# Kernel tuning notes

Measured on AMD Instinct MI355X. Metric: run time of the kernel, lower is better.

## Reference

```python
import jax, jax.numpy as jnp
import numpy as np

CTX = 2048   # context_window
D   = 256    # emb_dim
B   = 16     # batch
C   = 2048   # sequence length (<= CTX)


def make_rotary_matrix(ctx, d):
    """Dense per-position rotation matrix, as in the tinyllama get_rotary_matrix:
    theta_i = 10000 ** (-2*(i-1)/d), 2x2 rotation blocks on the diagonal."""
    pos = np.arange(ctx, dtype=np.float64)[:, None]            # [ctx, 1]
    i = np.arange(d // 2, dtype=np.float64)                    # [d/2]
    theta = 10000.0 ** (-2.0 * (i - 1.0) / d)                  # note (i-1), matches source
    ang = pos * theta                                          # [ctx, d/2]
    c, s = np.cos(ang), np.sin(ang)
    R = np.zeros((ctx, d, d), dtype=np.float32)
    k = np.arange(d // 2)
    R[:, 2 * k, 2 * k] = c
    R[:, 2 * k, 2 * k + 1] = -s
    R[:, 2 * k + 1, 2 * k] = s
    R[:, 2 * k + 1, 2 * k + 1] = c
    return jnp.asarray(R)


def setup_inputs() -> dict:
    key = jax.random.key(0)
    ks = jax.random.split(key, 4)
    scale = 1.0 / np.sqrt(D)
    x = jax.random.normal(ks[0], (B, C, D), dtype=jnp.float32)
    Wq = jax.random.normal(ks[1], (D, D), dtype=jnp.float32) * scale
    Wk = jax.random.normal(ks[2], (D, D), dtype=jnp.float32) * scale
    Wv = jax.random.normal(ks[3], (D, D), dtype=jnp.float32) * scale
    bq = jnp.zeros((D,), dtype=jnp.float32)
    bk = jnp.zeros((D,), dtype=jnp.float32)
    bv = jnp.zeros((D,), dtype=jnp.float32)
    R = make_rotary_matrix(CTX, D)
    return {"x": x, "Wq": Wq, "bq": bq, "Wk": Wk, "bk": bk, "Wv": Wv, "bv": bv, "R": R}


def reference(x, Wq, bq, Wk, bk, Wv, bv, R):
    Bz, Cz, d = x.shape
    # QKV projections (torch Linear: y = x @ W.T + b)
    q = x @ Wq.T + bq
    k = x @ Wk.T + bk
    v = x @ Wv.T + bv
    # Dense rotary: q_rot[b,c,:] = R[c] @ q[b,c,:]  (original: bmm(q^T, R[:C]^T)^T)
    Rc = R[:Cz]                                        # [C, D, D]
    q_rot = jnp.einsum('bcd,ced->bce', q, Rc)          # [B, C, D]
    k_rot = jnp.einsum('bcd,ced->bce', k, Rc)          # [B, C, D]
    # Causal SDPA (dropout_p=0.2 in source -> disabled here, eval-mode determinism)
    scale = 1.0 / jnp.sqrt(jnp.asarray(d, dtype=x.dtype))
    scores = jnp.einsum('bqd,bkd->bqk', q_rot, k_rot) * scale   # [B, C, C]
    causal = jnp.tril(jnp.ones((Cz, Cz), dtype=bool))
    scores = jnp.where(causal, scores, jnp.asarray(-jnp.inf, dtype=scores.dtype))
    attn = jax.nn.softmax(scores, axis=-1)
    out = jnp.einsum('bqk,bkd->bqd', attn, v)                   # [B, C, D]
    return out
```

## Files before the change

kernel.cpp:

```cpp
#include <hip/hip_runtime.h>
#include <stdint.h>

#define BB 16
#define CC 2048
#define DD 256
#define MM (BB*CC)

typedef __attribute__((ext_vector_type(4))) float f32x4;
typedef __attribute__((ext_vector_type(8))) short bf16x8;
typedef __attribute__((ext_vector_type(4))) short s16x4;

static __device__ __forceinline__ short f2bf(float f) {
  union { float f; uint32_t u; } v; v.f = f;
  uint32_t u = v.u;
  return (short)((u + 0x7FFFu + ((u >> 16) & 1u)) >> 16);
}

#define GLDS16(gp, lp) __builtin_amdgcn_global_load_lds(                      \
    (const __attribute__((address_space(1))) void*)(gp),                      \
    (__attribute__((address_space(3))) void*)(lp), 16, 0, 0)

#define DPP_ROR_F(x, n) __uint_as_float(__builtin_amdgcn_update_dpp(          \
    0, (int)__float_as_uint(x), 0x120 + (n), 0xF, 0xF, false))

__global__ __launch_bounds__(256) void k_trig(float2* __restrict__ cs) {
  int id = blockIdx.x * 256 + threadIdx.x;
  int k = id & 127, pg = id >> 7;
  double th = pow(10000.0, (1.0 - (double)k) * (1.0 / 128.0));
  const double TWO_PI = 6.283185307179586476925287;
  const double INV_2PI = 1.0 / TWO_PI;
  #pragma unroll
  for (int i = 0; i < 16; ++i) {
    int pos = pg * 16 + i;
    double ang = (double)pos * th;
    double red = ang - floor(ang * INV_2PI) * TWO_PI;
    float fr = (float)red;
    cs[(size_t)pos * 128 + k] = make_float2(__cosf(fr), __sinf(fr));
  }
}

__global__ __launch_bounds__(256) void k_wconv(
    const float* __restrict__ Wq, const float* __restrict__ Wk,
    const float* __restrict__ Wv, short* __restrict__ wb) {
  int gid = blockIdx.x * 256 + threadIdx.x;
  int mat = gid >> 14;
  int rem = gid & 16383;
  int kc = rem >> 11;
  int o  = (rem & 2047) * 8;
  int e  = o >> 6;
  int c4 = ((o & 63) ^ (((e >> 1) & 3) << 4)) >> 3;
  const float* W = (mat == 0) ? Wq : (mat == 1) ? Wk : Wv;
  f32x4 wv = *(const f32x4*)(W + (size_t)e * DD + kc * 32 + c4 * 4);
  s16x4 b4;
  b4[0] = f2bf(wv[0]); b4[1] = f2bf(wv[1]); b4[2] = f2bf(wv[2]); b4[3] = f2bf(wv[3]);
  *(s16x4*)((char*)wb + (size_t)gid * 8) = b4;
}

__global__ __launch_bounds__(256, 2) void k_qkv(
    const float* __restrict__ x, const short* __restrict__ wb,
    const float* __restrict__ bq, const float* __restrict__ bk,
    const float* __restrict__ bv, const float2* __restrict__ cs,
    short* __restrict__ q_rot, short* __restrict__ k_rot,
    short* __restrict__ v_t)
{
  __shared__ char SM[32768 + 49152];
  short* xs = (short*)SM;
  char* wsh = SM + 32768;
  const int t = threadIdx.x;
  const int lane = t & 63, w = t >> 6;
  const int g = lane >> 4, li = lane & 15;
  const int m0 = blockIdx.x * 64;

  #pragma unroll
  for (int i = 0; i < 16; ++i) {
    int chunk = i * 256 + t;
    int row = chunk >> 6, c4 = chunk & 63;
    f32x4 xv = *(const f32x4*)(x + (size_t)(m0 + row) * DD + c4 * 4);
    s16x4 b4;
    b4[0] = f2bf(xv[0]); b4[1] = f2bf(xv[1]); b4[2] = f2bf(xv[2]); b4[3] = f2bf(xv[3]);
    *(s16x4*)((char*)xs + row * 512 + ((c4 * 8) ^ ((row & 7) << 4))) = b4;
  }
  __syncthreads();

  f32x4 zero4 = {0.f, 0.f, 0.f, 0.f};
  f32x4 accQ[16], accK[16], accV[16];
  #pragma unroll
  for (int nt = 0; nt < 16; ++nt) { accQ[nt] = zero4; accK[nt] = zero4; accV[nt] = zero4; }

  for (int kc = 0; kc < 8; ++kc) {
    #pragma unroll
    for (int i = 0; i < 12; ++i) {
      int cc = i * 4 + w;
      const char* src = (const char*)wb + (size_t)(cc >> 4) * 131072 +
                        kc * 16384 + (cc & 15) * 1024 + lane * 16;
      GLDS16(src, wsh + cc * 1024);
    }
    asm volatile("s_waitcnt vmcnt(0)" ::: "memory");
    __builtin_amdgcn_sched_barrier(0);
    __builtin_amdgcn_s_barrier();

    const int arow = w * 16 + li;
    bf16x8 a = *(const bf16x8*)((char*)xs + arow * 512 +
                                (((kc * 64) + g * 16) ^ ((arow & 7) << 4)));
    #pragma unroll
    for (int nt = 0; nt < 16; ++nt) {
      int e = nt * 16 + li;
      int off = e * 64 + ((g * 16) ^ (((e >> 1) & 3) << 4));
      bf16x8 fq = *(const bf16x8*)(wsh + off);
      bf16x8 fk = *(const bf16x8*)(wsh + 16384 + off);
      bf16x8 fv = *(const bf16x8*)(wsh + 32768 + off);
      accQ[nt] = __builtin_amdgcn_mfma_f32_16x16x32_bf16(a, fq, accQ[nt], 0, 0, 0);
      accK[nt] = __builtin_amdgcn_mfma_f32_16x16x32_bf16(a, fk, accK[nt], 0, 0, 0);
      accV[nt] = __builtin_amdgcn_mfma_f32_16x16x32_bf16(a, fv, accV[nt], 0, 0, 0);
    }
    __builtin_amdgcn_s_barrier();
  }

  __syncthreads();
  {
    char* Tq = SM;
    char* Tk = SM + 33792;
    #pragma unroll
    for (int nt = 0; nt < 16; ++nt) {
      int e = nt * 16 + li;
      float bQ = bq[e], bK = bk[e];
      #pragma unroll
      for (int r = 0; r < 4; ++r) {
        int cloc = w * 16 + g * 4 + r;
        int m = m0 + cloc;
        float2 csv = cs[(size_t)(m & (CC - 1)) * 128 + (e >> 1)];
        float vq = accQ[nt][r] + bQ;
        float oq = __shfl_xor(vq, 1);
        vq = csv.x * vq + ((e & 1) ? csv.y * oq : -csv.y * oq);
        *(short*)(Tq + cloc * 528 + e * 2) = f2bf(vq * 0.0625f);
        float vk = accK[nt][r] + bK;
        float ok = __shfl_xor(vk, 1);
        vk = csv.x * vk + ((e & 1) ? csv.y * ok : -csv.y * ok);
        *(short*)(Tk + cloc * 528 + e * 2) = f2bf(vk);
      }
    }
    __syncthreads();
    #pragma unroll
    for (int it = 0; it < 8; ++it) {
      int chunk = it * 256 + t;
      int c = chunk >> 5, e32 = chunk & 31;
      int4 vq4 = *(const int4*)(Tq + c * 528 + e32 * 16);
      int4 vk4 = *(const int4*)(Tk + c * 528 + e32 * 16);
      *(int4*)(q_rot + (size_t)(m0 + c) * DD + e32 * 8) = vq4;
      *(int4*)(k_rot + (size_t)(m0 + c) * DD + e32 * 8) = vk4;
    }
  }
  __syncthreads();
  #pragma unroll
  for (int nt = 0; nt < 16; ++nt) {
    int e = nt * 16 + li;
    float bias = bv[e];
    #pragma unroll
    for (int r = 0; r < 4; ++r) {
      int cloc = w * 16 + g * 4 + r;
      *(short*)(SM + e * 144 + cloc * 2) = f2bf(accV[nt][r] + bias);
    }
  }
  __syncthreads();
  {
    const int bb = m0 >> 11, c0 = m0 & (CC - 1);
    #pragma unroll
    for (int it = 0; it < 8; ++it) {
      int chunk = it * 256 + t;
      int e = chunk >> 3, c8 = chunk & 7;
      int4 vv = *(const int4*)(SM + e * 144 + c8 * 16);
      *(int4*)(v_t + ((size_t)(bb * DD + e)) * CC + c0 + c8 * 8) = vv;
    }
  }
}

__global__ __launch_bounds__(512, 2) void k_attn(
    const short* __restrict__ q_rot, const short* __restrict__ k_rot,
    const short* __restrict__ v_t, float* __restrict__ out)
{
  __shared__ char SM[143360];
  const int t = threadIdx.x;
  const int lane = t & 63, w = t >> 6;
  const int wg = w & 3, gq = w >> 2;
  const int g = lane >> 4, li = lane & 15;

  const int p = blockIdx.x;
  const int b = p & 15;
  const int j = p >> 4;

  const short* kbase = k_rot + (size_t)b * CC * DD;
  const short* vbase = v_t  + (size_t)b * DD * CC;

  float* U  = (float*)(SM + 65536);
  float* ML = (float*)(SM + 142848);
  char* Pb = SM + 132608 + w * 1280;

  f32x4 zero4 = {0.f, 0.f, 0.f, 0.f};

  for (int tt = 0; tt < 2; ++tt) {
    const int qt = tt ? (31 - j) : j;
    const int q0 = qt * 64;
    const int NTg = qt + 1;
    const int kvoff = gq * 32 * NTg;

    const short* qb = q_rot + ((size_t)b * CC + q0 + wg * 16 + li) * DD;
    bf16x8 qf[8];
    #pragma unroll
    for (int dc = 0; dc < 8; ++dc)
      qf[dc] = *(const bf16x8*)(qb + dc * 32 + g * 8);

    f32x4 O[16];
    #pragma unroll
    for (int i = 0; i < 16; ++i) O[i] = zero4;
    float mrow[4], lrow[4];
    #pragma unroll
    for (int r = 0; r < 4; ++r) { mrow[r] = -__builtin_inff(); lrow[r] = 0.f; }

    auto STAGE = [&](int buf, int kt) {
      const int k0s = kvoff + kt * 32;
      char* dst = SM + (size_t)(gq * 2 + buf) * 32768;
      #pragma unroll
      for (int i = 0; i < 4; ++i) {
        int c = i * 4 + wg;
        int row = 2 * c + (lane >> 5);
        int cb = ((lane & 31) * 16) ^ ((row & 7) << 4);
        const char* src = (const char*)(kbase + (size_t)(k0s + row) * DD) + cb;
        GLDS16(src, dst + c * 1024);
      }
      #pragma unroll
      for (int i = 0; i < 4; ++i) {
        int c = i * 4 + wg;
        int d = 16 * c + (lane >> 2);
        int sb = (((lane & 3) ^ ((lane >> 3) & 3)) * 16);
        const char* src = (const char*)(vbase + (size_t)d * CC + k0s) + sb;
        GLDS16(src, dst + 16384 + c * 1024);
      }
    };

    int cur = 0;
    STAGE(0, 0);
    for (int kt = 0; kt < NTg; ++kt) {
      const int k0 = kvoff + kt * 32;
      if (kt + 1 < NTg) {
        STAGE(cur ^ 1, kt + 1);
        asm volatile("s_waitcnt vmcnt(8)" ::: "memory");
      } else {
        asm volatile("s_waitcnt vmcnt(0)" ::: "memory");
      }
      __builtin_amdgcn_sched_barrier(0);
      __builtin_amdgcn_s_barrier();

      const char* Kb = SM + (size_t)(gq * 2 + cur) * 32768;
      const char* Vb = Kb + 16384;

      f32x4 S[2];
      S[0] = zero4; S[1] = zero4;
      __builtin_amdgcn_s_setprio(1);
      #pragma unroll
      for (int dc = 0; dc < 8; ++dc) {
        #pragma unroll
        for (int nt = 0; nt < 2; ++nt) {
          int krow = nt * 16 + li;
          bf16x8 kf = *(const bf16x8*)(Kb + krow * 512 +
                                       (((dc * 64) + g * 16) ^ ((krow & 7) << 4)));
          S[nt] = __builtin_amdgcn_mfma_f32_16x16x32_bf16(qf[dc], kf, S[nt], 0, 0, 0);
        }
      }
      __builtin_amdgcn_s_setprio(0);

      if (k0 + 31 > q0) {
        #pragma unroll
        for (int nt = 0; nt < 2; ++nt)
          #pragma unroll
          for (int r = 0; r < 4; ++r)
            if ((k0 + nt * 16 + li) > (q0 + wg * 16 + g * 4 + r))
              S[nt][r] = -1.0e30f;
      }

      float mxr[4];
      #pragma unroll
      for (int r = 0; r < 4; ++r) {
        float mx = fmaxf(S[0][r], S[1][r]);
        mx = fmaxf(mx, DPP_ROR_F(mx, 8));
        mx = fmaxf(mx, DPP_ROR_F(mx, 4));
        mx = fmaxf(mx, DPP_ROR_F(mx, 2));
        mx = fmaxf(mx, DPP_ROR_F(mx, 1));
        mxr[r] = mx;
      }
      int need = 0;
      #pragma unroll
      for (int r = 0; r < 4; ++r) need |= (mxr[r] > mrow[r] + 8.f) ? 1 : 0;
      if (__any(need)) {
        #pragma unroll
        for (int r = 0; r < 4; ++r) {
          float mnew = fmaxf(mrow[r], mxr[r]);
          float al = __expf(mrow[r] - mnew);
          mrow[r] = mnew;
          lrow[r] *= al;
          #pragma unroll
          for (int dt2 = 0; dt2 < 16; ++dt2) O[dt2][r] *= al;
        }
      }
      #pragma unroll
      for (int r = 0; r < 4; ++r) {
        float rsum = 0.f;
        #pragma unroll
        for (int nt = 0; nt < 2; ++nt) {
          float pv = __expf(S[nt][r] - mrow[r]);
          S[nt][r] = pv;
          rsum += pv;
        }
        rsum += DPP_ROR_F(rsum, 8);
        rsum += DPP_ROR_F(rsum, 4);
        rsum += DPP_ROR_F(rsum, 2);
        rsum += DPP_ROR_F(rsum, 1);
        lrow[r] += rsum;
      }

      #pragma unroll
      for (int nt = 0; nt < 2; ++nt)
        #pragma unroll
        for (int r = 0; r < 4; ++r)
          *(short*)(Pb + (g * 4 + r) * 80 + (nt * 16 + li) * 2) = f2bf(S[nt][r]);

      bf16x8 pf = *(const bf16x8*)(Pb + li * 80 + g * 16);

      __builtin_amdgcn_s_setprio(1);
      #pragma unroll
      for (int dt2 = 0; dt2 < 16; ++dt2) {
        bf16x8 vf = *(const bf16x8*)(Vb + (dt2 * 16 + li) * 64 +
                                     ((g * 16) ^ ((((li) >> 1) & 3) << 4)));
        O[dt2] = __builtin_amdgcn_mfma_f32_16x16x32_bf16(pf, vf, O[dt2], 0, 0, 0);
      }
      __builtin_amdgcn_s_setprio(0);

      __builtin_amdgcn_s_barrier();
      cur ^= 1;
    }

    __syncthreads();
    if (gq == 1) {
      #pragma unroll
      for (int r = 0; r < 4; ++r) {
        int row = wg * 16 + g * 4 + r;
        if (li == 0) { ML[row * 2] = mrow[r]; ML[row * 2 + 1] = lrow[r]; }
        #pragma unroll
        for (int dt2 = 0; dt2 < 16; ++dt2)
          U[row * 260 + dt2 * 16 + li] = O[dt2][r];
      }
    }
    __syncthreads();
    if (gq == 0) {
      float eA[4], eB[4], invl[4];
      #pragma unroll
      for (int r = 0; r < 4; ++r) {
        int row = wg * 16 + g * 4 + r;
        float mB = ML[row * 2], lB = ML[row * 2 + 1];
        float m = fmaxf(mrow[r], mB);
        eA[r] = __expf(mrow[r] - m);
        eB[r] = __expf(mB - m);
        invl[r] = 1.f / (lrow[r] * eA[r] + lB * eB[r]);
      }
      #pragma unroll
      for (int dt2 = 0; dt2 < 16; ++dt2)
        #pragma unroll
        for (int r = 0; r < 4; ++r) {
          int row = wg * 16 + g * 4 + r;
          float uB = U[row * 260 + dt2 * 16 + li];
          out[((size_t)b * CC + q0 + row) * DD + dt2 * 16 + li] =
              (O[dt2][r] * eA[r] + uB * eB[r]) * invl[r];
        }
    }
    __syncthreads();
  }
}

extern "C" void kernel_launch(void* const* d_in, const int* in_sizes, int n_in,
                              void* d_out, int out_size, void* d_ws, size_t ws_size,
                              hipStream_t stream) {
  const float* x  = (const float*)d_in[0];
  const float* Wq = (const float*)d_in[1];
  const float* bq = (const float*)d_in[2];
  const float* Wk = (const float*)d_in[3];
  const float* bk = (const float*)d_in[4];
  const float* Wv = (const float*)d_in[5];
  const float* bv = (const float*)d_in[6];
  float* out = (float*)d_out;
  (void)in_sizes; (void)n_in; (void)out_size; (void)ws_size;

  char* ws = (char*)d_ws;
  float2* cs   = (float2*)ws;
  short* q_rot = (short*)(ws + (2u << 20));
  short* k_rot = q_rot + (size_t)MM * DD;
  short* v_tr  = k_rot + (size_t)MM * DD;
  short* wb    = v_tr + (size_t)MM * DD;

  k_trig <<<  64, 256, 0, stream>>>(cs);
  k_wconv<<< 192, 256, 0, stream>>>(Wq, Wk, Wv, wb);
  k_qkv  <<< 512, 256, 0, stream>>>(x, wb, bq, bk, bv, cs, q_rot, k_rot, v_tr);
  k_attn <<< 256, 512, 0, stream>>>(q_rot, k_rot, v_tr, out);
}
```

Measured before the change: 129.3 us.

## Split QKV projection across six waves, one matrix per wave pair

The QKV kernel grows from 4 to 6 waves per block. Each pair of waves owns one of Q, K, V and computes 32 rows by 256 columns, instead of each wave computing all three matrices for 16 rows. This cuts accumulator registers per wave (32 instead of 48 f32x4) and reuses each weight fragment across two row blocks. The LDS-staged transpose and store epilogue is replaced by direct scattered 2-byte global stores for q/k and 8-byte stores for v_t, which drops barriers but may lower store coalescing.

```diff
diff --git a/kernel.cpp b/kernel.cpp
--- a/kernel.cpp
+++ b/kernel.cpp
@@ -56,7 +56,7 @@
   *(s16x4*)((char*)wb + (size_t)gid * 8) = b4;
 }
 
-__global__ __launch_bounds__(256, 2) void k_qkv(
+__global__ __launch_bounds__(384, 2) void k_qkv(
     const float* __restrict__ x, const short* __restrict__ wb,
     const float* __restrict__ bq, const float* __restrict__ bk,
     const float* __restrict__ bv, const float2* __restrict__ cs,
@@ -68,29 +68,34 @@
   char* wsh = SM + 32768;
   const int t = threadIdx.x;
   const int lane = t & 63, w = t >> 6;
+  const int mat = w >> 1, h = w & 1;
   const int g = lane >> 4, li = lane & 15;
   const int m0 = blockIdx.x * 64;
 
   #pragma unroll
-  for (int i = 0; i < 16; ++i) {
-    int chunk = i * 256 + t;
-    int row = chunk >> 6, c4 = chunk & 63;
-    f32x4 xv = *(const f32x4*)(x + (size_t)(m0 + row) * DD + c4 * 4);
-    s16x4 b4;
-    b4[0] = f2bf(xv[0]); b4[1] = f2bf(xv[1]); b4[2] = f2bf(xv[2]); b4[3] = f2bf(xv[3]);
-    *(s16x4*)((char*)xs + row * 512 + ((c4 * 8) ^ ((row & 7) << 4))) = b4;
+  for (int i = 0; i < 11; ++i) {
+    int chunk = i * 384 + t;
+    if (chunk < 4096) {
+      int row = chunk >> 6, c4 = chunk & 63;
+      f32x4 xv = *(const f32x4*)(x + (size_t)(m0 + row) * DD + c4 * 4);
+      s16x4 b4;
+      b4[0] = f2bf(xv[0]); b4[1] = f2bf(xv[1]); b4[2] = f2bf(xv[2]); b4[3] = f2bf(xv[3]);
+      *(s16x4*)((char*)xs + row * 512 + ((c4 * 8) ^ ((row & 7) << 4))) = b4;
+    }
   }
   __syncthreads();
 
   f32x4 zero4 = {0.f, 0.f, 0.f, 0.f};
-  f32x4 accQ[16], accK[16], accV[16];
+  f32x4 acc[2][16];
   #pragma unroll
-  for (int nt = 0; nt < 16; ++nt) { accQ[nt] = zero4; accK[nt] = zero4; accV[nt] = zero4; }
+  for (int rb = 0; rb < 2; ++rb)
+    #pragma unroll
+    for (int nt = 0; nt < 16; ++nt) acc[rb][nt] = zero4;
 
   for (int kc = 0; kc < 8; ++kc) {
     #pragma unroll
-    for (int i = 0; i < 12; ++i) {
-      int cc = i * 4 + w;
+    for (int i = 0; i < 8; ++i) {
+      int cc = i * 6 + w;
       const char* src = (const char*)wb + (size_t)(cc >> 4) * 131072 +
                         kc * 16384 + (cc & 15) * 1024 + lane * 16;
       GLDS16(src, wsh + cc * 1024);
@@ -99,77 +104,59 @@
     __builtin_amdgcn_sched_barrier(0);
     __builtin_amdgcn_s_barrier();
 
-    const int arow = w * 16 + li;
-    bf16x8 a = *(const bf16x8*)((char*)xs + arow * 512 +
-                                (((kc * 64) + g * 16) ^ ((arow & 7) << 4)));
+    bf16x8 a[2];
+    #pragma unroll
+    for (int rb = 0; rb < 2; ++rb) {
+      int arow = h * 32 + rb * 16 + li;
+      a[rb] = *(const bf16x8*)((char*)xs + arow * 512 +
+                               (((kc * 64) + g * 16) ^ ((arow & 7) << 4)));
+    }
     #pragma unroll
     for (int nt = 0; nt < 16; ++nt) {
       int e = nt * 16 + li;
-      int off = e * 64 + ((g * 16) ^ (((e >> 1) & 3) << 4));
-      bf16x8 fq = *(const bf16x8*)(wsh + off);
-      bf16x8 fk = *(const bf16x8*)(wsh + 16384 + off);
-      bf16x8 fv = *(const bf16x8*)(wsh + 32768 + off);
-      accQ[nt] = __builtin_amdgcn_mfma_f32_16x16x32_bf16(a, fq, accQ[nt], 0, 0, 0);
-      accK[nt] = __builtin_amdgcn_mfma_f32_16x16x32_bf16(a, fk, accK[nt], 0, 0, 0);
-      accV[nt] = __builtin_amdgcn_mfma_f32_16x16x32_bf16(a, fv, accV[nt], 0, 0, 0);
+      int off = mat * 16384 + e * 64 + ((g * 16) ^ (((e >> 1) & 3) << 4));
+      bf16x8 f = *(const bf16x8*)(wsh + off);
+      acc[0][nt] = __builtin_amdgcn_mfma_f32_16x16x32_bf16(a[0], f, acc[0][nt], 0, 0, 0);
+      acc[1][nt] = __builtin_amdgcn_mfma_f32_16x16x32_bf16(a[1], f, acc[1][nt], 0, 0, 0);
     }
     __builtin_amdgcn_s_barrier();
   }
 
-  __syncthreads();
-  {
-    char* Tq = SM;
-    char* Tk = SM + 33792;
+  if (mat < 2) {
+    short* dst = mat ? k_rot : q_rot;
+    const float* bias_p = mat ? bk : bq;
+    const float qs = mat ? 1.0f : 0.0625f;
     #pragma unroll
     for (int nt = 0; nt < 16; ++nt) {
       int e = nt * 16 + li;
-      float bQ = bq[e], bK = bk[e];
-      #pragma unroll
-      for (int r = 0; r < 4; ++r) {
-        int cloc = w * 16 + g * 4 + r;
-        int m = m0 + cloc;
-        float2 csv = cs[(size_t)(m & (CC - 1)) * 128 + (e >> 1)];
-        float vq = accQ[nt][r] + bQ;
-        float oq = __shfl_xor(vq, 1);
-        vq = csv.x * vq + ((e & 1) ? csv.y * oq : -csv.y * oq);
-        *(short*)(Tq + cloc * 528 + e * 2) = f2bf(vq * 0.0625f);
-        float vk = accK[nt][r] + bK;
-        float ok = __shfl_xor(vk, 1);
-        vk = csv.x * vk + ((e & 1) ? csv.y * ok : -csv.y * ok);
-        *(short*)(Tk + cloc * 528 + e * 2) = f2bf(vk);
-      }
-    }
-    __syncthreads();
-    #pragma unroll
-    for (int it = 0; it < 8; ++it) {
-      int chunk = it * 256 + t;
-      int c = chunk >> 5, e32 = chunk & 31;
-      int4 vq4 = *(const int4*)(Tq + c * 528 + e32 * 16);
-      int4 vk4 = *(const int4*)(Tk + c * 528 + e32 * 16);
-      *(int4*)(q_rot + (size_t)(m0 + c) * DD + e32 * 8) = vq4;
-      *(int4*)(k_rot + (size_t)(m0 + c) * DD + e32 * 8) = vk4;
-    }
-  }
-  __syncthreads();
-  #pragma unroll
-  for (int nt = 0; nt < 16; ++nt) {
-    int e = nt * 16 + li;
-    float bias = bv[e];
-    #pragma unroll
-    for (int r = 0; r < 4; ++r) {
-      int cloc = w * 16 + g * 4 + r;
-      *(short*)(SM + e * 144 + cloc * 2) = f2bf(accV[nt][r] + bias);
-    }
-  }
-  __syncthreads();
-  {
+      float bias = bias_p[e];
+      #pragma unroll
+      for (int rb = 0; rb < 2; ++rb) {
+        #pragma unroll
+        for (int r = 0; r < 4; ++r) {
+          int m = m0 + h * 32 + rb * 16 + g * 4 + r;
+          float2 csv = cs[(size_t)(m & (CC - 1)) * 128 + (e >> 1)];
+          float val = acc[rb][nt][r] + bias;
+          float other = __shfl_xor(val, 1);
+          val = csv.x * val + ((e & 1) ? csv.y * other : -csv.y * other);
+          dst[(size_t)m * DD + e] = f2bf(val * qs);
+        }
+      }
+    }
+  } else {
     const int bb = m0 >> 11, c0 = m0 & (CC - 1);
     #pragma unroll
-    for (int it = 0; it < 8; ++it) {
-      int chunk = it * 256 + t;
-      int e = chunk >> 3, c8 = chunk & 7;
-      int4 vv = *(const int4*)(SM + e * 144 + c8 * 16);
-      *(int4*)(v_t + ((size_t)(bb * DD + e)) * CC + c0 + c8 * 8) = vv;
+    for (int nt = 0; nt < 16; ++nt) {
+      int e = nt * 16 + li;
+      float bias = bv[e];
+      #pragma unroll
+      for (int rb = 0; rb < 2; ++rb) {
+        s16x4 o4;
+        #pragma unroll
+        for (int r = 0; r < 4; ++r) o4[r] = f2bf(acc[rb][nt][r] + bias);
+        int c = c0 + h * 32 + rb * 16 + g * 4;
+        *(s16x4*)(v_t + ((size_t)(bb * DD + e)) * CC + c) = o4;
+      }
     }
   }
 }
@@ -397,6 +384,6 @@
 
   k_trig <<<  64, 256, 0, stream>>>(cs);
   k_wconv<<< 192, 256, 0, stream>>>(Wq, Wk, Wv, wb);
-  k_qkv  <<< 512, 256, 0, stream>>>(x, wb, bq, bk, bv, cs, q_rot, k_rot, v_tr);
+  k_qkv  <<< 512, 384, 0, stream>>>(x, wb, bq, bk, bv, cs, q_rot, k_rot, v_tr);
   k_attn <<< 256, 512, 0, stream>>>(q_rot, k_rot, v_tr, out);
 }
```

Result: slower. 137.2 us (+6.1%).

## Repartition attention waves to 32 query rows by half head-dim each

Applied to the files above, without the earlier changes.

Each wave in a KV group now owns 32 query rows (two 16-row blocks) and half of the 256-wide output dimension, where before it owned 16 rows and the full width. Each K fragment read from LDS now feeds two MFMAs and each V fragment feeds two, halving LDS fragment traffic per MFMA in the PV stage. In exchange, QK^T and softmax are computed redundantly by the two waves that share a query-row pair, which doubles QK MFMA work. The P scratch buffer also grows.

```diff
diff --git a/kernel.cpp b/kernel.cpp
--- a/kernel.cpp
+++ b/kernel.cpp
@@ -178,10 +178,11 @@
     const short* __restrict__ q_rot, const short* __restrict__ k_rot,
     const short* __restrict__ v_t, float* __restrict__ out)
 {
-  __shared__ char SM[143360];
+  __shared__ char SM[153600];
   const int t = threadIdx.x;
   const int lane = t & 63, w = t >> 6;
   const int wg = w & 3, gq = w >> 2;
+  const int qs = wg & 1, dh = wg >> 1;
   const int g = lane >> 4, li = lane & 15;
 
   const int p = blockIdx.x;
@@ -192,8 +193,8 @@
   const short* vbase = v_t  + (size_t)b * DD * CC;
 
   float* U  = (float*)(SM + 65536);
-  float* ML = (float*)(SM + 142848);
-  char* Pb = SM + 132608 + w * 1280;
+  float* ML = (float*)(SM + 153088);
+  char* Pb = SM + 132608 + w * 2560;
 
   f32x4 zero4 = {0.f, 0.f, 0.f, 0.f};
 
@@ -203,18 +204,25 @@
     const int NTg = qt + 1;
     const int kvoff = gq * 32 * NTg;
 
-    const short* qb = q_rot + ((size_t)b * CC + q0 + wg * 16 + li) * DD;
-    bf16x8 qf[8];
-    #pragma unroll
-    for (int dc = 0; dc < 8; ++dc)
-      qf[dc] = *(const bf16x8*)(qb + dc * 32 + g * 8);
-
-    f32x4 O[16];
-    #pragma unroll
-    for (int i = 0; i < 16; ++i) O[i] = zero4;
-    float mrow[4], lrow[4];
-    #pragma unroll
-    for (int r = 0; r < 4; ++r) { mrow[r] = -__builtin_inff(); lrow[r] = 0.f; }
+    bf16x8 qf[2][8];
+    #pragma unroll
+    for (int rb = 0; rb < 2; ++rb) {
+      const short* qb = q_rot + ((size_t)b * CC + q0 + qs * 32 + rb * 16 + li) * DD;
+      #pragma unroll
+      for (int dc = 0; dc < 8; ++dc)
+        qf[rb][dc] = *(const bf16x8*)(qb + dc * 32 + g * 8);
+    }
+
+    f32x4 O[2][8];
+    #pragma unroll
+    for (int rb = 0; rb < 2; ++rb)
+      #pragma unroll
+      for (int i = 0; i < 8; ++i) O[rb][i] = zero4;
+    float mrow[2][4], lrow[2][4];
+    #pragma unroll
+    for (int rb = 0; rb < 2; ++rb)
+      #pragma unroll
+      for (int r = 0; r < 4; ++r) { mrow[rb][r] = -__builtin_inff(); lrow[rb][r] = 0.f; }
 
     auto STAGE = [&](int buf, int kt) {
       const int k0s = kvoff + kt * 32;
@@ -253,8 +261,9 @@
       const char* Kb = SM + (size_t)(gq * 2 + cur) * 32768;
       const char* Vb = Kb + 16384;
 
-      f32x4 S[2];
-      S[0] = zero4; S[1] = zero4;
+      f32x4 S[2][2];
+      #pragma unroll
+      for (int rb = 0; rb < 2; ++rb) { S[rb][0] = zero4; S[rb][1] = zero4; }
       __builtin_amdgcn_s_setprio(1);
       #pragma unroll
       for (int dc = 0; dc < 8; ++dc) {
@@ -263,74 +272,91 @@
           int krow = nt * 16 + li;
           bf16x8 kf = *(const bf16x8*)(Kb + krow * 512 +
                                        (((dc * 64) + g * 16) ^ ((krow & 7) << 4)));
-          S[nt] = __builtin_amdgcn_mfma_f32_16x16x32_bf16(qf[dc], kf, S[nt], 0, 0, 0);
+          S[0][nt] = __builtin_amdgcn_mfma_f32_16x16x32_bf16(qf[0][dc], kf, S[0][nt], 0, 0, 0);
+          S[1][nt] = __builtin_amdgcn_mfma_f32_16x16x32_bf16(qf[1][dc], kf, S[1][nt], 0, 0, 0);
         }
       }
       __builtin_amdgcn_s_setprio(0);
 
       if (k0 + 31 > q0) {
         #pragma unroll
+        for (int rb = 0; rb < 2; ++rb)
+          #pragma unroll
+          for (int nt = 0; nt < 2; ++nt)
+            #pragma unroll
+            for (int r = 0; r < 4; ++r)
+              if ((k0 + nt * 16 + li) > (q0 + qs * 32 + rb * 16 + g * 4 + r))
+                S[rb][nt][r] = -1.0e30f;
+      }
+
+      float mxr[2][4];
+      #pragma unroll
+      for (int rb = 0; rb < 2; ++rb)
+        #pragma unroll
+        for (int r = 0; r < 4; ++r) {
+          float mx = fmaxf(S[rb][0][r], S[rb][1][r]);
+          mx = fmaxf(mx, DPP_ROR_F(mx, 8));
+          mx = fmaxf(mx, DPP_ROR_F(mx, 4));
+          mx = fmaxf(mx, DPP_ROR_F(mx, 2));
+          mx = fmaxf(mx, DPP_ROR_F(mx, 1));
+          mxr[rb][r] = mx;
+        }
+      int need = 0;
+      #pragma unroll
+      for (int rb = 0; rb < 2; ++rb)
+        #pragma unroll
+        for (int r = 0; r < 4; ++r) need |= (mxr[rb][r] > mrow[rb][r] + 8.f) ? 1 : 0;
+      if (__any(need)) {
+        #pragma unroll
+        for (int rb = 0; rb < 2; ++rb)
+          #pragma unroll
+          for (int r = 0; r < 4; ++r) {
+            float mnew = fmaxf(mrow[rb][r], mxr[rb][r]);
+            float al = __expf(mrow[rb][r] - mnew);
+            mrow[rb][r] = mnew;
+            lrow[rb][r] *= al;
+            #pragma unroll
+            for (int dt2 = 0; dt2 < 8; ++dt2) O[rb][dt2][r] *= al;
+          }
+      }
+      #pragma unroll
+      for (int rb = 0; rb < 2; ++rb)
+        #pragma unroll
+        for (int r = 0; r < 4; ++r) {
+          float rsum = 0.f;
+          #pragma unroll
+          for (int nt = 0; nt < 2; ++nt) {
+            float pv = __expf(S[rb][nt][r] - mrow[rb][r]);
+            S[rb][nt][r] = pv;
+            rsum += pv;
+          }
+          rsum += DPP_ROR_F(rsum, 8);
+          rsum += DPP_ROR_F(rsum, 4);
+          rsum += DPP_ROR_F(rsum, 2);
+          rsum += DPP_ROR_F(rsum, 1);
+          lrow[rb][r] += rsum;
+        }
+
+      #pragma unroll
+      for (int rb = 0; rb < 2; ++rb)
+        #pragma unroll
         for (int nt = 0; nt < 2; ++nt)
           #pragma unroll
           for (int r = 0; r < 4; ++r)
-            if ((k0 + nt * 16 + li) > (q0 + wg * 16 + g * 4 + r))
-              S[nt][r] = -1.0e30f;
-      }
-
-      float mxr[4];
-      #pragma unroll
-      for (int r = 0; r < 4; ++r) {
-        float mx = fmaxf(S[0][r], S[1][r]);
-        mx = fmaxf(mx, DPP_ROR_F(mx, 8));
-        mx = fmaxf(mx, DPP_ROR_F(mx, 4));
-        mx = fmaxf(mx, DPP_ROR_F(mx, 2));
-        mx = fmaxf(mx, DPP_ROR_F(mx, 1));
-        mxr[r] = mx;
-      }
-      int need = 0;
-      #pragma unroll
-      for (int r = 0; r < 4; ++r) need |= (mxr[r] > mrow[r] + 8.f) ? 1 : 0;
-      if (__any(need)) {
-        #pragma unroll
-        for (int r = 0; r < 4; ++r) {
-          float mnew = fmaxf(mrow[r], mxr[r]);
-          float al = __expf(mrow[r] - mnew);
-          mrow[r] = mnew;
-          lrow[r] *= al;
-          #pragma unroll
-          for (int dt2 = 0; dt2 < 16; ++dt2) O[dt2][r] *= al;
-        }
-      }
-      #pragma unroll
-      for (int r = 0; r < 4; ++r) {
-        float rsum = 0.f;
-        #pragma unroll
-        for (int nt = 0; nt < 2; ++nt) {
-          float pv = __expf(S[nt][r] - mrow[r]);
-          S[nt][r] = pv;
-          rsum += pv;
-        }
-        rsum += DPP_ROR_F(rsum, 8);
-        rsum += DPP_ROR_F(rsum, 4);
-        rsum += DPP_ROR_F(rsum, 2);
-        rsum += DPP_ROR_F(rsum, 1);
-        lrow[r] += rsum;
-      }
-
-      #pragma unroll
-      for (int nt = 0; nt < 2; ++nt)
-        #pragma unroll
-        for (int r = 0; r < 4; ++r)
-          *(short*)(Pb + (g * 4 + r) * 80 + (nt * 16 + li) * 2) = f2bf(S[nt][r]);
-
-      bf16x8 pf = *(const bf16x8*)(Pb + li * 80 + g * 16);
+            *(short*)(Pb + (rb * 16 + g * 4 + r) * 80 + (nt * 16 + li) * 2) =
+                f2bf(S[rb][nt][r]);
+
+      bf16x8 pf0 = *(const bf16x8*)(Pb + li * 80 + g * 16);
+      bf16x8 pf1 = *(const bf16x8*)(Pb + (16 + li) * 80 + g * 16);
 
       __builtin_amdgcn_s_setprio(1);
       #pragma unroll
-      for (int dt2 = 0; dt2 < 16; ++dt2) {
-        bf16x8 vf = *(const bf16x8*)(Vb + (dt2 * 16 + li) * 64 +
-                                     ((g * 16) ^ ((((li) >> 1) & 3) << 4)));
-        O[dt2] = __builtin_amdgcn_mfma_f32_16x16x32_bf16(pf, vf, O[dt2], 0, 0, 0);
+      for (int dt2 = 0; dt2 < 8; ++dt2) {
+        int d = dh * 128 + dt2 * 16 + li;
+        bf16x8 vf = *(const bf16x8*)(Vb + d * 64 +
+                                     ((g * 16) ^ (((li >> 1) & 3) << 4)));
+        O[0][dt2] = __builtin_amdgcn_mfma_f32_16x16x32_bf16(pf0, vf, O[0][dt2], 0, 0, 0);
+        O[1][dt2] = __builtin_amdgcn_mfma_f32_16x16x32_bf16(pf1, vf, O[1][dt2], 0, 0, 0);
       }
       __builtin_amdgcn_s_setprio(0);
 
@@ -341,35 +367,40 @@
     __syncthreads();
     if (gq == 1) {
       #pragma unroll
-      for (int r = 0; r < 4; ++r) {
-        int row = wg * 16 + g * 4 + r;
-        if (li == 0) { ML[row * 2] = mrow[r]; ML[row * 2 + 1] = lrow[r]; }
-        #pragma unroll
-        for (int dt2 = 0; dt2 < 16; ++dt2)
-          U[row * 260 + dt2 * 16 + li] = O[dt2][r];
-      }
+      for (int rb = 0; rb < 2; ++rb)
+        #pragma unroll
+        for (int r = 0; r < 4; ++r) {
+          int row = qs * 32 + rb * 16 + g * 4 + r;
+          if (li == 0 && dh == 0) { ML[row * 2] = mrow[rb][r]; ML[row * 2 + 1] = lrow[rb][r]; }
+          #pragma unroll
+          for (int dt2 = 0; dt2 < 8; ++dt2)
+            U[row * 260 + (dh * 8 + dt2) * 16 + li] = O[rb][dt2][r];
+        }
     }
     __syncthreads();
     if (gq == 0) {
-      float eA[4], eB[4], invl[4];
-      #pragma unroll
-      for (int r = 0; r < 4; ++r) {
-        int row = wg * 16 + g * 4 + r;
-        float mB = ML[row * 2], lB = ML[row * 2 + 1];
-        float m = fmaxf(mrow[r], mB);
-        eA[r] = __expf(mrow[r] - m);
-        eB[r] = __expf(mB - m);
-        invl[r] = 1.f / (lrow[r] * eA[r] + lB * eB[r]);
-      }
-      #pragma unroll
-      for (int dt2 = 0; dt2 < 16; ++dt2)
+      #pragma unroll
+      for (int rb = 0; rb < 2; ++rb) {
+        float eA[4], eB[4], invl[4];
         #pragma unroll
         for (int r = 0; r < 4; ++r) {
-          int row = wg * 16 + g * 4 + r;
-          float uB = U[row * 260 + dt2 * 16 + li];
-          out[((size_t)b * CC + q0 + row) * DD + dt2 * 16 + li] =
-              (O[dt2][r] * eA[r] + uB * eB[r]) * invl[r];
+          int row = qs * 32 + rb * 16 + g * 4 + r;
+          float mB = ML[row * 2], lB = ML[row * 2 + 1];
+          float m = fmaxf(mrow[rb][r], mB);
+          eA[r] = __expf(mrow[rb][r] - m);
+          eB[r] = __expf(mB - m);
+          invl[r] = 1.f / (lrow[rb][r] * eA[r] + lB * eB[r]);
         }
+        #pragma unroll
+        for (int dt2 = 0; dt2 < 8; ++dt2)
+          #pragma unroll
+          for (int r = 0; r < 4; ++r) {
+            int row = qs * 32 + rb * 16 + g * 4 + r;
+            float uB = U[row * 260 + (dh * 8 + dt2) * 16 + li];
+            out[((size_t)b * CC + q0 + row) * DD + dh * 128 + dt2 * 16 + li] =
+                (O[rb][dt2][r] * eA[r] + uB * eB[r]) * invl[r];
+          }
+      }
     }
     __syncthreads();
   }
```

Result: slower. 157.3 us (+21.6%).
